# Performance work log

Hardware: AMD Instinct MI355X
Metric: run time of the kernel (lower is better)

## Reference

```python
import jax, jax.numpy as jnp
import numpy as np

# pywt db8 reconstruction low-pass filter (rec_lo); other filters derived per pywt conventions
_REC_LO = np.array([
    0.05441584224308161, 0.3128715909144659, 0.6756307362980128,
    0.5853546836548691, -0.015829105256023893, -0.2840155429624281,
    0.00047248457399797254, 0.128747426620186, -0.01736930100202211,
    -0.04408825393106472, 0.013981027917015516, 0.008746094047015655,
    -0.00487035299301066, -0.0003917403729959771, 0.0006754494059985568,
    -0.00011747678400228192], dtype=np.float64)
_F = 16
_REC_HI = np.array([(-1.0) ** k * _REC_LO[_F - 1 - k] for k in range(_F)])  # qmf
_DEC_LO = _REC_LO[::-1].copy()
_DEC_HI = _REC_HI[::-1].copy()
# lax.conv does cross-correlation; np.convolve flips the filter, so pre-flip here
_DEC_K = np.ascontiguousarray(np.stack([_DEC_LO[::-1], _DEC_HI[::-1]])[:, None, :])  # [2,1,F]
_REC_K = np.ascontiguousarray(np.stack([_REC_LO[::-1], _REC_HI[::-1]])[None, :, :])  # [1,2,F]
_THRESHOLD_FACTOR = 1.0


def _dwt_last(x):
    # single-level DWT along last axis, pywt 'symmetric' boundary mode
    shp = x.shape
    xf = x.reshape(-1, 1, shp[-1])
    xe = jnp.pad(xf, ((0, 0), (0, 0), (_F - 1, _F - 1)), mode='symmetric')[:, :, 1:]
    y = jax.lax.conv_general_dilated(xe, jnp.asarray(_DEC_K, x.dtype), (2,), 'VALID',
                                     dimension_numbers=('NCW', 'OIW', 'NCW'))  # [M,2,n]
    n = y.shape[-1]  # n = floor((N + F - 1) / 2)
    return y[:, 0].reshape(shp[:-1] + (n,)), y[:, 1].reshape(shp[:-1] + (n,))


def _idwt_last(ca, cd, out_len):
    # single-level inverse DWT along last axis; out_len = 2*n - F + 2
    shp = ca.shape
    n = shp[-1]
    m = int(np.prod(shp[:-1]))
    u = jnp.zeros((m, 2, 2 * n), ca.dtype)
    u = u.at[:, 0, ::2].set(ca.reshape(m, n)).at[:, 1, ::2].set(cd.reshape(m, n))
    ue = jnp.pad(u, ((0, 0), (0, 0), (_F - 1, _F - 1)))
    y = jax.lax.conv_general_dilated(ue, jnp.asarray(_REC_K, ca.dtype), (1,), 'VALID',
                                     dimension_numbers=('NCW', 'OIW', 'NCW'))[:, 0]
    return y[:, _F - 2:_F - 2 + out_len].reshape(shp[:-1] + (out_len,))


def _forward(x):
    B, H, W, C = x.shape
    M = B * C
    xm = jnp.transpose(x, (0, 3, 1, 2)).reshape(M, H, W)
    # level-1 wavedec2: rows (W axis) then columns (H axis)
    lo, hi = _dwt_last(xm)                               # [M,H,nW]
    ll, lh = _dwt_last(jnp.swapaxes(lo, -1, -2))         # [M,nW,nH]
    hl, hh = _dwt_last(jnp.swapaxes(hi, -1, -2))         # [M,nW,nH]
    # universal threshold from median abs of all detail subbands, per sample/channel
    det = jnp.concatenate([lh.reshape(M, -1), hl.reshape(M, -1), hh.reshape(M, -1)], axis=-1)
    sigma = jnp.median(jnp.abs(det), axis=-1) / 0.6745
    t = (sigma * jnp.sqrt(2.0 * jnp.log(float(H * W))) * _THRESHOLD_FACTOR)[:, None, None]
    soft = lambda c: jnp.sign(c) * jnp.maximum(jnp.abs(c) - t, 0.0)
    lh, hl, hh = soft(lh), soft(hl), soft(hh)
    # waverec2: inverse along H then along W
    nH = ll.shape[-1]
    Hr = 2 * nH - _F + 2
    rl = jnp.swapaxes(_idwt_last(ll, lh, Hr), -1, -2)    # [M,Hr,nW]
    rh = jnp.swapaxes(_idwt_last(hl, hh, Hr), -1, -2)    # [M,Hr,nW]
    nW = rl.shape[-1]
    y = _idwt_last(rl, rh, 2 * nW - _F + 2)              # [M,Hr,Wr]
    y = y[:, :H, :W].reshape(B, C, H, W)
    return jnp.transpose(y, (0, 2, 3, 1)).astype(x.dtype)


def setup_inputs() -> dict:
    key = jax.random.key(0)
    x = jax.random.normal(key, (32, 512, 512, 3), dtype=jnp.float32)
    return {"x": x}


def reference(x):
    return _forward(x)
```

## Files before the change

kernel.cpp:

```cpp
#include <hip/hip_runtime.h>
#include <math.h>

#define B_   32
#define H_   512
#define W_   512
#define C_   3
#define M_   96
#define NW_  263
#define NH_  263
#define DETPER 69169
#define DETTOT 207507
#define DETSTRIDE 207508
#define NVEC 51876
#define KRANK  103753u

#define SXS 144
#define CR  12

#define NBY   16
#define SLICE 2048

__device__ __constant__ float RLO[16] = {
    0.05441584224308161f,  0.3128715909144659f,   0.6756307362980128f,
    0.5853546836548691f,  -0.015829105256023893f, -0.2840155429624281f,
    0.00047248457399797254f, 0.128747426620186f,  -0.01736930100202211f,
   -0.04408825393106472f,  0.013981027917015516f,  0.008746094047015655f,
   -0.00487035299301066f, -0.0003917403729959771f, 0.0006754494059985568f,
   -0.00011747678400228192f};
__device__ __constant__ float RHI[16] = {
   -0.00011747678400228192f, -0.0006754494059985568f, -0.0003917403729959771f,
    0.00487035299301066f,     0.008746094047015655f,  -0.013981027917015516f,
   -0.04408825393106472f,     0.01736930100202211f,    0.128747426620186f,
   -0.00047248457399797254f, -0.2840155429624281f,     0.015829105256023893f,
    0.5853546836548691f,     -0.6756307362980128f,     0.3128715909144659f,
   -0.05441584224308161f};

__device__ __forceinline__ int refl(int q, int N) {
    if (q < 0)  return -q - 1;
    if (q >= N) return 2 * N - 1 - q;
    return q;
}

__device__ __forceinline__ float softthr(float v, float thr) {
    float a = fabsf(v) - thr;
    return a > 0.f ? copysignf(a, v) : 0.f;
}

__global__ __launch_bounds__(256) void k_zero(unsigned* __restrict__ p, int n) {
    int i = blockIdx.x * 256 + threadIdx.x;
    if (i < n) p[i] = 0u;
}

__global__ __launch_bounds__(256) void k_fwd(const float* __restrict__ x,
                                             float* __restrict__ ll,
                                             float* __restrict__ det) {
    __shared__ float sX[CR * SXS];
    __shared__ float sLO[46 * 64], sHI[46 * 64];
    const int m   = blockIdx.x;
    const int jw0 = blockIdx.y * 64;
    const int jh0 = blockIdx.z * 16;
    const int b = m / 3, c = m - 3 * (m / 3);
    const int tid = threadIdx.x;
    const int prow0 = 2 * jh0 - 14, pcol0 = 2 * jw0 - 14;
    for (int r0 = 0; r0 < 46; r0 += CR) {
        const int nr = (46 - r0) < CR ? (46 - r0) : CR;
        for (int l = tid; l < nr * 142; l += 256) {
            int rr = l / 142, cl = l - rr * 142;
            int h = refl(prow0 + r0 + rr, H_);
            int w = refl(pcol0 + cl, W_);
            sX[rr * SXS + cl] = x[((size_t)(b * H_ + h) * W_ + w) * C_ + c];
        }
        __syncthreads();
        for (int l = tid; l < nr * 64; l += 256) {
            int rr = l >> 6, j = l & 63;
            const float* px = &sX[rr * SXS + 2 * j];
            float al = 0.f, ah = 0.f;
#pragma unroll
            for (int k = 0; k < 16; ++k) {
                al = fmaf(px[k], RLO[k], al);
                ah = fmaf(px[k], RHI[k], ah);
            }
            sLO[(r0 + rr) * 64 + j] = al;
            sHI[(r0 + rr) * 64 + j] = ah;
        }
        __syncthreads();
    }
    const int tx = tid & 63, tg = tid >> 6;
    const int jw = jw0 + tx;
    if (jw >= NW_) return;
    float vl[22], vh[22];
#pragma unroll
    for (int s = 0; s < 22; ++s) {
        int row = 8 * tg + s;
        vl[s] = sLO[row * 64 + tx];
        vh[s] = sHI[row * 64 + tx];
    }
    float* llp = ll + (size_t)m * DETPER;
    float* dp  = det + (size_t)m * DETSTRIDE;
#pragma unroll
    for (int d = 0; d < 4; ++d) {
        int jh = jh0 + 4 * tg + d;
        if (jh >= NH_) continue;
        float a0 = 0.f, a1 = 0.f, a2 = 0.f, a3 = 0.f;
#pragma unroll
        for (int k = 0; k < 16; ++k) {
            float fl = vl[2 * d + k], fh = vh[2 * d + k];
            a0 = fmaf(fl, RLO[k], a0);
            a1 = fmaf(fl, RHI[k], a1);
            a2 = fmaf(fh, RLO[k], a2);
            a3 = fmaf(fh, RHI[k], a3);
        }
        size_t o = (size_t)jh * NW_ + jw;
        llp[o] = a0;
        dp[o] = a1;
        dp[DETPER + o] = a2;
        dp[2 * DETPER + o] = a3;
    }
}

__global__ __launch_bounds__(256) void k_hist1(const float* __restrict__ det,
                                               unsigned* __restrict__ hist) {
    __shared__ unsigned h[2048];
    const int tid = threadIdx.x, m = blockIdx.x;
    for (int i = tid; i < 2048; i += 256) h[i] = 0u;
    __syncthreads();
    const float* dp = det + (size_t)m * DETSTRIDE;
    const float4* dp4 = (const float4*)dp;
    const int stride = gridDim.y * 256;
    for (int v = blockIdx.y * 256 + tid; v < NVEC; v += stride) {
        float4 f = dp4[v];
        atomicAdd(&h[__float_as_uint(fabsf(f.x)) >> 21], 1u);
        atomicAdd(&h[__float_as_uint(fabsf(f.y)) >> 21], 1u);
        atomicAdd(&h[__float_as_uint(fabsf(f.z)) >> 21], 1u);
        atomicAdd(&h[__float_as_uint(fabsf(f.w)) >> 21], 1u);
    }
    if (blockIdx.y == 0 && tid < DETTOT - 4 * NVEC) {
        unsigned u = __float_as_uint(fabsf(dp[4 * NVEC + tid]));
        atomicAdd(&h[u >> 21], 1u);
    }
    __syncthreads();
    for (int i = tid; i < 2048; i += 256)
        if (h[i]) atomicAdd(&hist[m * 2048 + i], h[i]);
}

__global__ __launch_bounds__(256) void k_hist2(const float* __restrict__ det,
                                               const int* __restrict__ selBin1,
                                               unsigned* __restrict__ hist,
                                               unsigned* __restrict__ cnt,
                                               unsigned* __restrict__ list,
                                               int docap) {
    __shared__ unsigned h[2048];
    __shared__ unsigned ccnt;
    const int tid = threadIdx.x, m = blockIdx.x, by = blockIdx.y;
    const unsigned target = (unsigned)selBin1[m];
    for (int i = tid; i < 2048; i += 256) h[i] = 0u;
    if (tid == 0) ccnt = 0u;
    __syncthreads();
    const float* dp = det + (size_t)m * DETSTRIDE;
    const float4* dp4 = (const float4*)dp;
    const int stride = gridDim.y * 256;
    unsigned* const lst = list + ((size_t)m * NBY + by) * SLICE;
    const unsigned lane = tid & 63;
    auto take = [&](unsigned u) {
        bool pred = ((u >> 21) == target);
        if (pred) atomicAdd(&h[(u >> 10) & 0x7FFu], 1u);
        if (docap) {
            unsigned long long mask = __ballot(pred);
            if (pred) {
                unsigned off = (unsigned)__popcll(mask & ((1ull << lane) - 1ull));
                int leader = __ffsll((unsigned long long)mask) - 1;
                unsigned base = 0u;
                if ((int)lane == leader)
                    base = atomicAdd(&ccnt, (unsigned)__popcll(mask));
                base = (unsigned)__shfl((int)base, leader, 64);
                unsigned p = base + off;
                if (p < SLICE) lst[p] = u;
            }
        }
    };
    for (int v = by * 256 + tid; v < NVEC; v += stride) {
        float4 f = dp4[v];
        take(__float_as_uint(fabsf(f.x)));
        take(__float_as_uint(fabsf(f.y)));
        take(__float_as_uint(fabsf(f.z)));
        take(__float_as_uint(fabsf(f.w)));
    }
    if (by == 0 && tid < DETTOT - 4 * NVEC)
        take(__float_as_uint(fabsf(dp[4 * NVEC + tid])));
    __syncthreads();
    if (docap && tid == 0) cnt[m * NBY + by] = ccnt;
    for (int i = tid; i < 2048; i += 256)
        if (h[i]) atomicAdd(&hist[m * 2048 + i], h[i]);
}

__global__ __launch_bounds__(256) void k_hist3(const float* __restrict__ det,
                                               const int* __restrict__ selBin1,
                                               const int* __restrict__ selBin2,
                                               const unsigned* __restrict__ cnt,
                                               const unsigned* __restrict__ list,
                                               int docap,
                                               unsigned* __restrict__ hist) {
    __shared__ unsigned h[1024];
    const int tid = threadIdx.x, m = blockIdx.x, by = blockIdx.y;
    for (int i = tid; i < 1024; i += 256) h[i] = 0u;
    __syncthreads();
    bool fast = (docap != 0);
    if (fast) {
#pragma unroll
        for (int i = 0; i < NBY; ++i)
            if (cnt[m * NBY + i] > SLICE) fast = false;
    }
    if (fast) {
        const unsigned b2 = (unsigned)selBin2[m];
        const unsigned n = cnt[m * NBY + by];
        const unsigned* lst = list + ((size_t)m * NBY + by) * SLICE;
        for (unsigned i = tid; i < n; i += 256) {
            unsigned u = lst[i];
            if (((u >> 10) & 0x7FFu) == b2) atomicAdd(&h[u & 0x3FFu], 1u);
        }
    } else {
        const unsigned target = ((unsigned)selBin1[m] << 11) | (unsigned)selBin2[m];
        const float* dp = det + (size_t)m * DETSTRIDE;
        const float4* dp4 = (const float4*)dp;
        const int stride = gridDim.y * 256;
        for (int v = by * 256 + tid; v < NVEC; v += stride) {
            float4 f = dp4[v];
            unsigned a = __float_as_uint(fabsf(f.x));
            unsigned b = __float_as_uint(fabsf(f.y));
            unsigned c = __float_as_uint(fabsf(f.z));
            unsigned d = __float_as_uint(fabsf(f.w));
            if ((a >> 10) == target) atomicAdd(&h[a & 0x3FFu], 1u);
            if ((b >> 10) == target) atomicAdd(&h[b & 0x3FFu], 1u);
            if ((c >> 10) == target) atomicAdd(&h[c & 0x3FFu], 1u);
            if ((d >> 10) == target) atomicAdd(&h[d & 0x3FFu], 1u);
        }
        if (by == 0 && tid < DETTOT - 4 * NVEC) {
            unsigned u = __float_as_uint(fabsf(dp[4 * NVEC + tid]));
            if ((u >> 10) == target) atomicAdd(&h[u & 0x3FFu], 1u);
        }
    }
    __syncthreads();
    for (int i = tid; i < 1024; i += 256)
        if (h[i]) atomicAdd(&hist[m * 1024 + i], h[i]);
}

__device__ int histSelect(unsigned* hist, int nb, unsigned rank, unsigned* rem) {
    __shared__ unsigned ps[256];
    __shared__ int s_bin;
    __shared__ unsigned s_rem;
    const int tid = threadIdx.x;
    if (tid == 0) { s_bin = 0; s_rem = 0; }
    const int per = nb >> 8;
    unsigned s = 0;
    for (int i = 0; i < per; ++i) s += hist[tid * per + i];
    ps[tid] = s;
    __syncthreads();
    for (int off = 1; off < 256; off <<= 1) {
        unsigned v = ps[tid];
        unsigned add = (tid >= off) ? ps[tid - off] : 0u;
        __syncthreads();
        ps[tid] = v + add;
        __syncthreads();
    }
    unsigned incl = ps[tid], excl = incl - s;
    if (rank >= excl && rank < incl) {
        unsigned cum = excl;
        for (int i = 0; i < per; ++i) {
            unsigned c = hist[tid * per + i];
            if (cum + c > rank) { s_bin = tid * per + i; s_rem = rank - cum; break; }
            cum += c;
        }
    }
    __syncthreads();
    int rbin = s_bin;
    unsigned rr = s_rem;
    __syncthreads();
    *rem = rr;
    return rbin;
}

__global__ __launch_bounds__(256) void k_sel2048(const unsigned* __restrict__ hist,
                                                 const unsigned* __restrict__ rankIn,
                                                 int* __restrict__ selBin,
                                                 unsigned* __restrict__ rankOut) {
    __shared__ unsigned h[2048];
    const int m = blockIdx.x, tid = threadIdx.x;
    for (int i = tid; i < 2048; i += 256) h[i] = hist[m * 2048 + i];
    __syncthreads();
    unsigned rank = rankIn ? rankIn[m] : KRANK;
    unsigned rem;
    int bin = histSelect(h, 2048, rank, &rem);
    if (tid == 0) { selBin[m] = bin; rankOut[m] = rem; }
}

__global__ __launch_bounds__(256) void k_sel3(const unsigned* __restrict__ hist,
                                              const unsigned* __restrict__ rankIn,
                                              const int* __restrict__ selBin1,
                                              const int* __restrict__ selBin2,
                                              float* __restrict__ tval) {
    __shared__ unsigned h[1024];
    const int m = blockIdx.x, tid = threadIdx.x;
    for (int i = tid; i < 1024; i += 256) h[i] = hist[m * 1024 + i];
    __syncthreads();
    unsigned rem;
    int low = histSelect(h, 1024, rankIn[m], &rem);
    if (tid == 0) {
        unsigned bits = ((unsigned)selBin1[m] << 21) | ((unsigned)selBin2[m] << 10) | (unsigned)low;
        double med = (double)__uint_as_float(bits);
        tval[m] = (float)(med / 0.6745 * 4.995327667046959);
    }
}

__global__ __launch_bounds__(256) void k_inv(const float* __restrict__ ll,
                                             const float* __restrict__ det,
                                             const float* __restrict__ tval,
                                             float* __restrict__ out) {
    __shared__ float sLL[23 * 40], sLH[23 * 40], sHL[23 * 40], sHH[23 * 40];
    __shared__ float sRL[32 * 40], sRH[32 * 40];
    const int m  = blockIdx.x;
    const int w0 = blockIdx.y * 64;
    const int t0 = blockIdx.z * 32;
    const int b = m / 3, c = m - 3 * (m / 3);
    const int tid = threadIdx.x;
    const float thr = tval[m];
    const int jW0 = w0 >> 1, s0 = t0 >> 1;
    const float* llp = ll + (size_t)m * DETPER;
    const float* dp  = det + (size_t)m * DETSTRIDE;
    for (int l = tid; l < 23 * 39; l += 256) {
        int rr = l / 39, cc = l - rr * 39;
        size_t o = (size_t)(s0 + rr) * NW_ + (jW0 + cc);
        int li = rr * 40 + cc;
        sLL[li] = llp[o];
        sLH[li] = softthr(dp[o], thr);
        sHL[li] = softthr(dp[DETPER + o], thr);
        sHH[li] = softthr(dp[2 * DETPER + o], thr);
    }
    __syncthreads();
    for (int l = tid; l < 160; l += 256) {
        int s = l / 10, q = l - 10 * (l / 10);
        float4 aL0 = make_float4(0.f, 0.f, 0.f, 0.f), aL1 = aL0, aH0 = aL0, aH1 = aL0;
#pragma unroll
        for (int a = 0; a < 8; ++a) {
            int li = (s + 7 - a) * 40 + 4 * q;
            float4 vLL = *(const float4*)&sLL[li];
            float4 vLH = *(const float4*)&sLH[li];
            float4 vHL = *(const float4*)&sHL[li];
            float4 vHH = *(const float4*)&sHH[li];
            float w00 = RLO[2 * a],     h00 = RHI[2 * a];
            float w01 = RLO[2 * a + 1], h01 = RHI[2 * a + 1];
            aL0.x = fmaf(vLL.x, w00, fmaf(vLH.x, h00, aL0.x));
            aL0.y = fmaf(vLL.y, w00, fmaf(vLH.y, h00, aL0.y));
            aL0.z = fmaf(vLL.z, w00, fmaf(vLH.z, h00, aL0.z));
            aL0.w = fmaf(vLL.w, w00, fmaf(vLH.w, h00, aL0.w));
            aL1.x = fmaf(vLL.x, w01, fmaf(vLH.x, h01, aL1.x));
            aL1.y = fmaf(vLL.y, w01, fmaf(vLH.y, h01, aL1.y));
            aL1.z = fmaf(vLL.z, w01, fmaf(vLH.z, h01, aL1.z));
            aL1.w = fmaf(vLL.w, w01, fmaf(vLH.w, h01, aL1.w));
            aH0.x = fmaf(vHL.x, w00, fmaf(vHH.x, h00, aH0.x));
            aH0.y = fmaf(vHL.y, w00, fmaf(vHH.y, h00, aH0.y));
            aH0.z = fmaf(vHL.z, w00, fmaf(vHH.z, h00, aH0.z));
            aH0.w = fmaf(vHL.w, w00, fmaf(vHH.w, h00, aH0.w));
            aH1.x = fmaf(vHL.x, w01, fmaf(vHH.x, h01, aH1.x));
            aH1.y = fmaf(vHL.y, w01, fmaf(vHH.y, h01, aH1.y));
            aH1.z = fmaf(vHL.z, w01, fmaf(vHH.z, h01, aH1.z));
            aH1.w = fmaf(vHL.w, w01, fmaf(vHH.w, h01, aH1.w));
        }
        *(float4*)&sRL[(2 * s) * 40 + 4 * q]     = aL0;
        *(float4*)&sRL[(2 * s + 1) * 40 + 4 * q] = aL1;
        *(float4*)&sRH[(2 * s) * 40 + 4 * q]     = aH0;
        *(float4*)&sRH[(2 * s + 1) * 40 + 4 * q] = aH1;
    }
    __syncthreads();
    {
        const int tr = tid >> 3, jg = tid & 7;
        const float4* pl = (const float4*)&sRL[tr * 40 + 4 * jg];
        const float4* ph = (const float4*)&sRH[tr * 40 + 4 * jg];
        float4 L0 = pl[0], L1 = pl[1], L2 = pl[2];
        float4 K0 = ph[0], K1 = ph[1], K2 = ph[2];
        float rl[12] = {L0.x,L0.y,L0.z,L0.w, L1.x,L1.y,L1.z,L1.w, L2.x,L2.y,L2.z,L2.w};
        float rh[12] = {K0.x,K0.y,K0.z,K0.w, K1.x,K1.y,K1.z,K1.w, K2.x,K2.y,K2.z,K2.w};
        size_t obase = ((size_t)(b * H_ + (t0 + tr)) * W_ + (w0 + 8 * jg)) * C_ + c;
#pragma unroll
        for (int u = 0; u < 4; ++u) {
#pragma unroll
            for (int r = 0; r < 2; ++r) {
                float acc = 0.f;
#pragma unroll
                for (int a = 0; a < 8; ++a) {
                    int sdx = u + 7 - a;
                    acc = fmaf(rl[sdx], RLO[2 * a + r], fmaf(rh[sdx], RHI[2 * a + r], acc));
                }
                out[obase + (size_t)(2 * u + r) * C_] = acc;
            }
        }
    }
}

extern "C" void kernel_launch(void* const* d_in, const int* in_sizes, int n_in,
                              void* d_out, int out_size, void* d_ws, size_t ws_size,
                              hipStream_t stream) {
    const float* x = (const float*)d_in[0];
    float* out = (float*)d_out;

    char* ws = (char*)d_ws;
    float* ll  = (float*)ws; ws += (size_t)M_ * DETPER * 4;
    float* det = (float*)ws; ws += (size_t)M_ * DETSTRIDE * 4;
    unsigned* hist1 = (unsigned*)ws; ws += (size_t)M_ * 2048 * 4;
    unsigned* hist2 = (unsigned*)ws; ws += (size_t)M_ * 2048 * 4;
    unsigned* hist3 = (unsigned*)ws; ws += (size_t)M_ * 1024 * 4;
    unsigned* cnt   = (unsigned*)ws;   ws += M_ * NBY * 4;
    int*      selBin1 = (int*)ws;      ws += M_ * 4;
    int*      selBin2 = (int*)ws;      ws += M_ * 4;
    unsigned* rank1   = (unsigned*)ws; ws += M_ * 4;
    unsigned* rank2   = (unsigned*)ws; ws += M_ * 4;
    float*    tval    = (float*)ws;    ws += M_ * 4;
    unsigned* list    = (unsigned*)ws; ws += (size_t)M_ * NBY * SLICE * 4;
    const int docap = (ws_size >= (size_t)(ws - (char*)d_ws)) ? 1 : 0;

    const int histWords = M_ * (2048 + 2048 + 1024) + M_ * NBY;
    k_zero   <<<dim3((histWords + 255) / 256), 256, 0, stream>>>(hist1, histWords);
    k_fwd    <<<dim3(M_, 5, 17),  256, 0, stream>>>(x, ll, det);
    k_hist1  <<<dim3(M_, NBY),    256, 0, stream>>>(det, hist1);
    k_sel2048<<<dim3(M_),         256, 0, stream>>>(hist1, nullptr, selBin1, rank1);
    k_hist2  <<<dim3(M_, NBY),    256, 0, stream>>>(det, selBin1, hist2, cnt, list, docap);
    k_sel2048<<<dim3(M_),         256, 0, stream>>>(hist2, rank1, selBin2, rank2);
    k_hist3  <<<dim3(M_, NBY),    256, 0, stream>>>(det, selBin1, selBin2, cnt, list, docap, hist3);
    k_sel3   <<<dim3(M_),         256, 0, stream>>>(hist3, rank2, selBin1, selBin2, tval);
    k_inv    <<<dim3(M_, 8, 16),  256, 0, stream>>>(ll, det, tval, out);
}
```

Measured before the change: 471.5 us.

## Use per-thread candidate lists in histogram passes and remap block indices for locality

The median-select histogram passes now give each thread its own slot in a strided candidate list instead of a per-block list filled through ballot, prefix count and a shared atomic. A per-channel overflow flag replaces the per-block count check. The forward and inverse kernels also remap the linear block index so the three channels of the same batch and tile run in adjacent blocks, which should improve cache reuse of the interleaved-channel input and output. The per-thread lists cost more workspace, and the fast path falls back to a full rescan for any channel where a thread overflows its capacity.

```diff
diff --git a/kernel.cpp b/kernel.cpp
--- a/kernel.cpp
+++ b/kernel.cpp
@@ -18,7 +18,8 @@
 #define CR  12
 
 #define NBY   16
-#define SLICE 2048
+#define SLOTS 4096
+#define SCAP  24
 
 __device__ __constant__ float RLO[16] = {
     0.05441584224308161f,  0.3128715909144659f,   0.6756307362980128f,
@@ -56,10 +57,14 @@
                                              float* __restrict__ det) {
     __shared__ float sX[CR * SXS];
     __shared__ float sLO[46 * 64], sHI[46 * 64];
-    const int m   = blockIdx.x;
-    const int jw0 = blockIdx.y * 64;
-    const int jh0 = blockIdx.z * 16;
-    const int b = m / 3, c = m - 3 * (m / 3);
+    const int lin = blockIdx.x + 96 * blockIdx.y + 480 * blockIdx.z;
+    const int q = lin >> 3, s = lin & 7;
+    const int c = q % 3, Thi = q / 3;
+    const int T = Thi * 8 + s;
+    const int b = T / 85, r = T - 85 * b;
+    const int jw0 = (r % 5) * 64;
+    const int jh0 = (r / 5) * 16;
+    const int m = 3 * b + c;
     const int tid = threadIdx.x;
     const int prow0 = 2 * jh0 - 14, pcol0 = 2 * jw0 - 14;
     for (int r0 = 0; r0 < 46; r0 += CR) {
@@ -90,10 +95,10 @@
     if (jw >= NW_) return;
     float vl[22], vh[22];
 #pragma unroll
-    for (int s = 0; s < 22; ++s) {
-        int row = 8 * tg + s;
-        vl[s] = sLO[row * 64 + tx];
-        vh[s] = sHI[row * 64 + tx];
+    for (int sr = 0; sr < 22; ++sr) {
+        int row = 8 * tg + sr;
+        vl[sr] = sLO[row * 64 + tx];
+        vh[sr] = sHI[row * 64 + tx];
     }
     float* llp = ll + (size_t)m * DETPER;
     float* dp  = det + (size_t)m * DETSTRIDE;
@@ -147,34 +152,26 @@
                                                const int* __restrict__ selBin1,
                                                unsigned* __restrict__ hist,
                                                unsigned* __restrict__ cnt,
+                                               unsigned* __restrict__ ovf,
                                                unsigned* __restrict__ list,
                                                int docap) {
     __shared__ unsigned h[2048];
-    __shared__ unsigned ccnt;
     const int tid = threadIdx.x, m = blockIdx.x, by = blockIdx.y;
     const unsigned target = (unsigned)selBin1[m];
     for (int i = tid; i < 2048; i += 256) h[i] = 0u;
-    if (tid == 0) ccnt = 0u;
     __syncthreads();
     const float* dp = det + (size_t)m * DETSTRIDE;
     const float4* dp4 = (const float4*)dp;
     const int stride = gridDim.y * 256;
-    unsigned* const lst = list + ((size_t)m * NBY + by) * SLICE;
-    const unsigned lane = tid & 63;
+    const unsigned slot = (unsigned)(by * 256 + tid);
+    unsigned* const lst = list + (size_t)m * SLOTS * SCAP;
+    unsigned mycnt = 0u;
     auto take = [&](unsigned u) {
-        bool pred = ((u >> 21) == target);
-        if (pred) atomicAdd(&h[(u >> 10) & 0x7FFu], 1u);
-        if (docap) {
-            unsigned long long mask = __ballot(pred);
-            if (pred) {
-                unsigned off = (unsigned)__popcll(mask & ((1ull << lane) - 1ull));
-                int leader = __ffsll((unsigned long long)mask) - 1;
-                unsigned base = 0u;
-                if ((int)lane == leader)
-                    base = atomicAdd(&ccnt, (unsigned)__popcll(mask));
-                base = (unsigned)__shfl((int)base, leader, 64);
-                unsigned p = base + off;
-                if (p < SLICE) lst[p] = u;
+        if ((u >> 21) == target) {
+            atomicAdd(&h[(u >> 10) & 0x7FFu], 1u);
+            if (docap) {
+                if (mycnt < SCAP) lst[mycnt * SLOTS + slot] = u;
+                ++mycnt;
             }
         }
     };
@@ -187,8 +184,11 @@
     }
     if (by == 0 && tid < DETTOT - 4 * NVEC)
         take(__float_as_uint(fabsf(dp[4 * NVEC + tid])));
-    __syncthreads();
-    if (docap && tid == 0) cnt[m * NBY + by] = ccnt;
+    if (docap) {
+        cnt[m * SLOTS + slot] = mycnt;
+        if (mycnt > SCAP) atomicOr(&ovf[m], 1u);
+    }
+    __syncthreads();
     for (int i = tid; i < 2048; i += 256)
         if (h[i]) atomicAdd(&hist[m * 2048 + i], h[i]);
 }
@@ -197,6 +197,7 @@
                                                const int* __restrict__ selBin1,
                                                const int* __restrict__ selBin2,
                                                const unsigned* __restrict__ cnt,
+                                               const unsigned* __restrict__ ovf,
                                                const unsigned* __restrict__ list,
                                                int docap,
                                                unsigned* __restrict__ hist) {
@@ -204,18 +205,14 @@
     const int tid = threadIdx.x, m = blockIdx.x, by = blockIdx.y;
     for (int i = tid; i < 1024; i += 256) h[i] = 0u;
     __syncthreads();
-    bool fast = (docap != 0);
-    if (fast) {
-#pragma unroll
-        for (int i = 0; i < NBY; ++i)
-            if (cnt[m * NBY + i] > SLICE) fast = false;
-    }
+    const bool fast = docap && (ovf[m] == 0u);
     if (fast) {
         const unsigned b2 = (unsigned)selBin2[m];
-        const unsigned n = cnt[m * NBY + by];
-        const unsigned* lst = list + ((size_t)m * NBY + by) * SLICE;
-        for (unsigned i = tid; i < n; i += 256) {
-            unsigned u = lst[i];
+        const unsigned slot = (unsigned)(by * 256 + tid);
+        const unsigned n = cnt[m * SLOTS + slot];
+        const unsigned* lst = list + (size_t)m * SLOTS * SCAP;
+        for (unsigned j = 0; j < n; ++j) {
+            unsigned u = lst[j * SLOTS + slot];
             if (((u >> 10) & 0x7FFu) == b2) atomicAdd(&h[u & 0x3FFu], 1u);
         }
     } else {
@@ -317,10 +314,14 @@
                                              float* __restrict__ out) {
     __shared__ float sLL[23 * 40], sLH[23 * 40], sHL[23 * 40], sHH[23 * 40];
     __shared__ float sRL[32 * 40], sRH[32 * 40];
-    const int m  = blockIdx.x;
-    const int w0 = blockIdx.y * 64;
-    const int t0 = blockIdx.z * 32;
-    const int b = m / 3, c = m - 3 * (m / 3);
+    const int lin = blockIdx.x + 96 * blockIdx.y + 768 * blockIdx.z;
+    const int qq = lin >> 3, s = lin & 7;
+    const int c = qq % 3, Uhi = qq / 3;
+    const int U = Uhi * 8 + s;
+    const int b = U >> 7, r = U & 127;
+    const int w0 = (r & 7) * 64;
+    const int t0 = (r >> 3) * 32;
+    const int m = 3 * b + c;
     const int tid = threadIdx.x;
     const float thr = tval[m];
     const int jW0 = w0 >> 1, s0 = t0 >> 1;
@@ -337,11 +338,11 @@
     }
     __syncthreads();
     for (int l = tid; l < 160; l += 256) {
-        int s = l / 10, q = l - 10 * (l / 10);
+        int s2 = l / 10, q = l - 10 * (l / 10);
         float4 aL0 = make_float4(0.f, 0.f, 0.f, 0.f), aL1 = aL0, aH0 = aL0, aH1 = aL0;
 #pragma unroll
         for (int a = 0; a < 8; ++a) {
-            int li = (s + 7 - a) * 40 + 4 * q;
+            int li = (s2 + 7 - a) * 40 + 4 * q;
             float4 vLL = *(const float4*)&sLL[li];
             float4 vLH = *(const float4*)&sLH[li];
             float4 vHL = *(const float4*)&sHL[li];
@@ -365,10 +366,10 @@
             aH1.z = fmaf(vHL.z, w01, fmaf(vHH.z, h01, aH1.z));
             aH1.w = fmaf(vHL.w, w01, fmaf(vHH.w, h01, aH1.w));
         }
-        *(float4*)&sRL[(2 * s) * 40 + 4 * q]     = aL0;
-        *(float4*)&sRL[(2 * s + 1) * 40 + 4 * q] = aL1;
-        *(float4*)&sRH[(2 * s) * 40 + 4 * q]     = aH0;
-        *(float4*)&sRH[(2 * s + 1) * 40 + 4 * q] = aH1;
+        *(float4*)&sRL[(2 * s2) * 40 + 4 * q]     = aL0;
+        *(float4*)&sRL[(2 * s2 + 1) * 40 + 4 * q] = aL1;
+        *(float4*)&sRH[(2 * s2) * 40 + 4 * q]     = aH0;
+        *(float4*)&sRH[(2 * s2 + 1) * 40 + 4 * q] = aH1;
     }
     __syncthreads();
     {
@@ -381,16 +382,16 @@
         float rh[12] = {K0.x,K0.y,K0.z,K0.w, K1.x,K1.y,K1.z,K1.w, K2.x,K2.y,K2.z,K2.w};
         size_t obase = ((size_t)(b * H_ + (t0 + tr)) * W_ + (w0 + 8 * jg)) * C_ + c;
 #pragma unroll
-        for (int u = 0; u < 4; ++u) {
-#pragma unroll
-            for (int r = 0; r < 2; ++r) {
+        for (int u2 = 0; u2 < 4; ++u2) {
+#pragma unroll
+            for (int rp = 0; rp < 2; ++rp) {
                 float acc = 0.f;
 #pragma unroll
                 for (int a = 0; a < 8; ++a) {
-                    int sdx = u + 7 - a;
-                    acc = fmaf(rl[sdx], RLO[2 * a + r], fmaf(rh[sdx], RHI[2 * a + r], acc));
+                    int sdx = u2 + 7 - a;
+                    acc = fmaf(rl[sdx], RLO[2 * a + rp], fmaf(rh[sdx], RHI[2 * a + rp], acc));
                 }
-                out[obase + (size_t)(2 * u + r) * C_] = acc;
+                out[obase + (size_t)(2 * u2 + rp) * C_] = acc;
             }
         }
     }
@@ -408,23 +409,24 @@
     unsigned* hist1 = (unsigned*)ws; ws += (size_t)M_ * 2048 * 4;
     unsigned* hist2 = (unsigned*)ws; ws += (size_t)M_ * 2048 * 4;
     unsigned* hist3 = (unsigned*)ws; ws += (size_t)M_ * 1024 * 4;
-    unsigned* cnt   = (unsigned*)ws;   ws += M_ * NBY * 4;
+    unsigned* ovf   = (unsigned*)ws;   ws += M_ * 4;
     int*      selBin1 = (int*)ws;      ws += M_ * 4;
     int*      selBin2 = (int*)ws;      ws += M_ * 4;
     unsigned* rank1   = (unsigned*)ws; ws += M_ * 4;
     unsigned* rank2   = (unsigned*)ws; ws += M_ * 4;
     float*    tval    = (float*)ws;    ws += M_ * 4;
-    unsigned* list    = (unsigned*)ws; ws += (size_t)M_ * NBY * SLICE * 4;
+    unsigned* cnt     = (unsigned*)ws; ws += (size_t)M_ * SLOTS * 4;
+    unsigned* list    = (unsigned*)ws; ws += (size_t)M_ * SLOTS * SCAP * 4;
     const int docap = (ws_size >= (size_t)(ws - (char*)d_ws)) ? 1 : 0;
 
-    const int histWords = M_ * (2048 + 2048 + 1024) + M_ * NBY;
+    const int histWords = M_ * (2048 + 2048 + 1024) + M_;
     k_zero   <<<dim3((histWords + 255) / 256), 256, 0, stream>>>(hist1, histWords);
     k_fwd    <<<dim3(M_, 5, 17),  256, 0, stream>>>(x, ll, det);
     k_hist1  <<<dim3(M_, NBY),    256, 0, stream>>>(det, hist1);
     k_sel2048<<<dim3(M_),         256, 0, stream>>>(hist1, nullptr, selBin1, rank1);
-    k_hist2  <<<dim3(M_, NBY),    256, 0, stream>>>(det, selBin1, hist2, cnt, list, docap);
+    k_hist2  <<<dim3(M_, NBY),    256, 0, stream>>>(det, selBin1, hist2, cnt, ovf, list, docap);
     k_sel2048<<<dim3(M_),         256, 0, stream>>>(hist2, rank1, selBin2, rank2);
-    k_hist3  <<<dim3(M_, NBY),    256, 0, stream>>>(det, selBin1, selBin2, cnt, list, docap, hist3);
+    k_hist3  <<<dim3(M_, NBY),    256, 0, stream>>>(det, selBin1, selBin2, cnt, ovf, list, docap, hist3);
     k_sel3   <<<dim3(M_),         256, 0, stream>>>(hist3, rank2, selBin1, selBin2, tval);
     k_inv    <<<dim3(M_, 8, 16),  256, 0, stream>>>(ll, det, tval, out);
 }
```

Result: slower. 482.0 us (+2.2%).
